# Optimization experiments

Measured on AMD Instinct MI355X. Metric: run time of the kernel, lower is better.

The kernel has to match this reference:

```python
import jax, jax.numpy as jnp
import numpy as np

LAMDA = 0.5
TEMPERATURE = 0.07
EPS = 1e-5


def setup_inputs() -> dict:
    key = jax.random.key(0)
    k1, k2, k3 = jax.random.split(key, 3)
    N, D = 8192, 128
    features = jax.random.normal(k1, (N, D), dtype=jnp.float32)
    labels = jax.random.randint(k2, (N,), 0, 100, dtype=jnp.int64 if jax.config.jax_enable_x64 else jnp.int32)
    domain_labels = jax.random.randint(k3, (N,), 0, 4, dtype=jnp.int64 if jax.config.jax_enable_x64 else jnp.int32)
    return {"features": features, "labels": labels, "domain_labels": domain_labels}


def reference(features, labels, domain_labels):
    N = features.shape[0]
    # L2-normalize rows (torch.nn.functional.normalize, eps=1e-12)
    norms = jnp.maximum(jnp.linalg.norm(features, axis=1, keepdims=True), 1e-12)
    f = features / norms
    sim = jnp.matmul(f, f.T) / TEMPERATURE  # [N, N]

    same_label = labels[:, None] == labels[None, :]
    same_dom = domain_labels[:, None] == domain_labels[None, :]
    offdiag = ~jnp.eye(N, dtype=bool)

    # per-pair domain weight: lamda in-domain, (1-lamda) out-of-domain
    w_exp = jnp.where(same_dom, LAMDA, 1.0 - LAMDA) * jnp.exp(sim)

    # denominator: all off-diagonal pairs (positives + negatives), weighted
    denom = jnp.sum(jnp.where(offdiag, w_exp, 0.0), axis=1) + EPS  # [N]

    pos = same_label & offdiag
    log_frac = jnp.log(w_exp / denom[:, None] + EPS)
    num_pos = jnp.sum(pos, axis=1)  # [N]
    loss_i = jnp.sum(jnp.where(pos, log_frac, 0.0), axis=1) / jnp.maximum(num_pos, 1)

    # anchors with zero positives produce NaN in torch and are skipped
    valid = num_pos > 0
    nans = jnp.sum(~valid)
    loss = -jnp.sum(jnp.where(valid, loss_i, 0.0))
    return loss / (N - nans + 1)
```

## Files before the change

### kernel.cpp

```cpp
#include <hip/hip_runtime.h>

#define NROWS 8192
#define DDIM  128
#define NBLK  (NROWS / 128)
#define NLAB  100
#define GCAP  160
#define GSPL  2
#define GTPB  5
#define EPSV  1e-5f
#define LN2F  0.69314718055994530942f
#define FSCALE 4.53981643f

typedef short s16x8 __attribute__((ext_vector_type(8)));
typedef float f32x4 __attribute__((ext_vector_type(4)));
typedef unsigned short u16;
typedef unsigned int u32;

__device__ __forceinline__ u16 f2bf(float x) {
  u32 b = __builtin_bit_cast(u32, x);
  u32 r = (b + 0x7FFFu + ((b >> 16) & 1u)) >> 16;
  return (u16)r;
}

__global__ __launch_bounds__(256) void norm_kernel(
    const float* __restrict__ feat, u16* __restrict__ g,
    float* __restrict__ denom) {
  int wave = threadIdx.x >> 6;
  int lane = threadIdx.x & 63;
  int row = (blockIdx.x << 2) + wave;
  const float* fr = feat + (size_t)row * DDIM + (lane << 1);
  float2 v = *(const float2*)fr;
  float ss = v.x * v.x + v.y * v.y;
#pragma unroll
  for (int m = 1; m < 64; m <<= 1) ss += __shfl_xor(ss, m);
  float inv = FSCALE / fmaxf(sqrtf(ss), 1e-12f);
  ushort2 o;
  o.x = f2bf(v.x * inv);
  o.y = f2bf(v.y * inv);
  *(ushort2*)(g + (size_t)row * DDIM + (lane << 1)) = o;
  if (lane == 0) denom[row] = 0.0f;
}

__global__ __launch_bounds__(1024) void bucket_kernel(
    const int* __restrict__ lab, int* __restrict__ offs,
    int* __restrict__ cnts, int* __restrict__ rowlist,
    float* __restrict__ Lsum) {
  __shared__ int h[NLAB], cur[NLAB], off[NLAB];
  int tid = threadIdx.x;
  if (tid < NLAB) h[tid] = 0;
  if (tid == 1023) *Lsum = 0.0f;
  __syncthreads();
  for (int i = tid; i < NROWS; i += 1024) atomicAdd(&h[lab[i]], 1);
  __syncthreads();
  if (tid == 0) {
    int s = 0;
    for (int l = 0; l < NLAB; ++l) { off[l] = s; s += h[l]; }
  }
  __syncthreads();
  if (tid < NLAB) { cur[tid] = off[tid]; offs[tid] = off[tid]; cnts[tid] = h[tid]; }
  __syncthreads();
  for (int i = tid; i < NROWS; i += 1024) {
    int p = atomicAdd(&cur[lab[i]], 1);
    rowlist[p] = i;
  }
}

#define LOADB_TO(bv, BsArr, jt)                                              \
  _Pragma("unroll")                                                          \
  for (int kc = 0; kc < 4; ++kc) {                                           \
    const int c_ = (kc << 2) + lh;                                           \
    bv[kc] = *(const s16x8*)(&BsArr[(size_t)((jt)*16 + lr) * DDIM +          \
                                    ((c_ ^ (lr & 7)) << 3)]);                \
  }

#define MFMA_TO(accv, bv, init0, init1)                                      \
  accv[0] = init0; accv[1] = init1;                                          \
  __builtin_amdgcn_s_setprio(1);                                             \
  _Pragma("unroll")                                                          \
  for (int kc = 0; kc < 4; ++kc) {                                           \
    accv[0] = __builtin_amdgcn_mfma_f32_16x16x32_bf16(a[0][kc], bv[kc],      \
                                                      accv[0], 0, 0, 0);     \
    accv[1] = __builtin_amdgcn_mfma_f32_16x16x32_bf16(a[1][kc], bv[kc],      \
                                                      accv[1], 0, 0, 0);     \
  }                                                                          \
  __builtin_amdgcn_s_setprio(0);

#define EPI_T(accv, jt)                                                      \
  {                                                                          \
    const int tj0 = j0 + (jt)*16;                                            \
    float csum = 0.f;                                                        \
    if (diagblk) {                                                           \
      _Pragma("unroll")                                                      \
      for (int rf = 0; rf < 2; ++rf)                                         \
      _Pragma("unroll")                                                      \
        for (int r = 0; r < 4; ++r) {                                        \
          float e_ = __builtin_amdgcn_exp2f(accv[rf][r]);                    \
          e_ = (gibase[rf] + r == tj0 + lr) ? 0.0f : e_;                     \
          dacc[rf][r] += e_;                                                 \
        }                                                                    \
    } else {                                                                 \
      _Pragma("unroll")                                                      \
      for (int rf = 0; rf < 2; ++rf)                                         \
      _Pragma("unroll")                                                      \
        for (int r = 0; r < 4; ++r) {                                        \
          float e_ = __builtin_amdgcn_exp2f(accv[rf][r]);                    \
          dacc[rf][r] += e_;                                                 \
          csum += e_;                                                        \
        }                                                                    \
      csum += __shfl_xor(csum, 16);                                          \
      csum += __shfl_xor(csum, 32);                                          \
      ccol[jt] = csum;                                                       \
    }                                                                        \
  }

__global__ __launch_bounds__(256, 4) void denom_tri(
    const u16* __restrict__ g, float* __restrict__ denom) {
  const int bi = blockIdx.x, bj = blockIdx.y;
  if (bj < bi) return;
  __shared__ u16 Bs[128 * DDIM];
  const int tid = threadIdx.x;
  const int wave = tid >> 6, lane = tid & 63;
  const int lr = lane & 15, lh = lane >> 4;
  const int i0 = bi * 128 + wave * 32;
  const int j0 = bj * 128;
  const bool diagblk = (bi == bj);

  {
    const int cs = (tid & 15) ^ ((tid >> 4) & 7);
#pragma unroll
    for (int k = 0; k < 8; ++k) {
      const u16* src = g + (size_t)(j0 + k * 16 + (tid >> 4)) * DDIM + (cs << 3);
      u16* dst = &Bs[(size_t)(k * 16 + (wave << 2)) * DDIM];
      __builtin_amdgcn_global_load_lds(
          (const __attribute__((address_space(1))) void*)src,
          (__attribute__((address_space(3))) void*)dst, 16, 0, 0);
    }
  }

  s16x8 a[2][4];
#pragma unroll
  for (int rf = 0; rf < 2; ++rf) {
    const u16* gr = g + (size_t)(i0 + rf * 16 + lr) * DDIM + lh * 8;
#pragma unroll
    for (int kc = 0; kc < 4; ++kc) a[rf][kc] = *(const s16x8*)(gr + kc * 32);
  }
  const int gibase[2] = {i0 + lh * 4, i0 + 16 + lh * 4};

  asm volatile("s_waitcnt vmcnt(0)" ::: "memory");
  __builtin_amdgcn_s_barrier();

  float dacc[2][4] = {};
  float ccol[8] = {};
  const f32x4 m1 = f32x4{-1.f, -1.f, -1.f, -1.f};

  s16x8 b0[4], b1[4];
  f32x4 acc0[2], acc1[2];

  LOADB_TO(b0, Bs, 0)
  MFMA_TO(acc0, b0, m1, m1)
#pragma unroll
  for (int p = 0; p < 3; ++p) {
    LOADB_TO(b1, Bs, 2 * p + 1)
    MFMA_TO(acc1, b1, m1, m1)
    EPI_T(acc0, 2 * p)
    LOADB_TO(b0, Bs, 2 * p + 2)
    MFMA_TO(acc0, b0, m1, m1)
    EPI_T(acc1, 2 * p + 1)
  }
  LOADB_TO(b1, Bs, 7)
  MFMA_TO(acc1, b1, m1, m1)
  EPI_T(acc0, 6)
  EPI_T(acc1, 7)

#pragma unroll
  for (int rf = 0; rf < 2; ++rf)
#pragma unroll
    for (int r = 0; r < 4; ++r) {
      float v = dacc[rf][r];
      v += __shfl_xor(v, 1); v += __shfl_xor(v, 2);
      v += __shfl_xor(v, 4); v += __shfl_xor(v, 8);
      if (lr == 0) atomicAdd(&denom[gibase[rf] + r], v);
    }
  if (!diagblk) {
#pragma unroll
    for (int jt = 0; jt < 8; ++jt)
      if (lane < 16) atomicAdd(&denom[j0 + jt * 16 + lane], ccol[jt]);
  }
}

__global__ __launch_bounds__(320) void group_loss(
    const u16* __restrict__ g, const int* __restrict__ offs,
    const int* __restrict__ cnts, const int* __restrict__ rowlist,
    const float* __restrict__ denom, float* __restrict__ Lsum) {
  __shared__ u16 Bs[GTPB * 16 * DDIM];
  const int lb = blockIdx.x;
  const int z = blockIdx.y;
  const int cnt = cnts[lb];
  if (cnt < 2) return;
  if (z * 16 >= cnt) return;
  const int off = offs[lb];
  const int tid = threadIdx.x;
  const int wave = tid >> 6, lane = tid & 63;
  const int lr = lane & 15, lh = lane >> 4;

#pragma unroll
  for (int s = 0; s < 4; ++s) {
    const int m = s * 320 + tid;
    const int rloc = m >> 4, cc = m & 15;
    const int jt_l = rloc >> 4, rr = rloc & 15;
    const int gidx = (jt_l * GSPL + z) * 16 + rr;
    const int cs = cc ^ (rloc & 7);
    const int grow = rowlist[off + (gidx < cnt ? gidx : 0)];
    const u16* src = g + (size_t)grow * DDIM + (cs << 3);
    u16* dst = &Bs[(size_t)(s * 320 + wave * 64) * 8];
    __builtin_amdgcn_global_load_lds(
        (const __attribute__((address_space(1))) void*)src,
        (__attribute__((address_space(3))) void*)dst, 16, 0, 0);
  }

  s16x8 a[2][4];
#pragma unroll
  for (int rf = 0; rf < 2; ++rf) {
    const int ar = wave * 32 + rf * 16 + lr;
    const int gar = rowlist[off + (ar < cnt ? ar : 0)];
    const u16* gr = g + (size_t)gar * DDIM + lh * 8;
#pragma unroll
    for (int kc = 0; kc < 4; ++kc) a[rf][kc] = *(const s16x8*)(gr + kc * 32);
  }
  const int erow[2] = {wave * 32 + lh * 4, wave * 32 + 16 + lh * 4};
  f32x4 cinit[2];
#pragma unroll
  for (int rf = 0; rf < 2; ++rf)
#pragma unroll
    for (int r = 0; r < 4; ++r) {
      const int er = erow[rf] + r;
      const int gi = rowlist[off + (er < cnt ? er : 0)];
      cinit[rf][r] = -__builtin_amdgcn_logf(denom[gi] + EPSV) - 1.0f;
    }

  asm volatile("s_waitcnt vmcnt(0)" ::: "memory");
  __builtin_amdgcn_s_barrier();

  float lacc[2][4] = {};

#pragma unroll
  for (int jt = 0; jt < GTPB; ++jt) {
    s16x8 b[4];
    LOADB_TO(b, Bs, jt)
    f32x4 acc[2];
    MFMA_TO(acc, b, cinit[0], cinit[1])
    const int col = (jt * GSPL + z) * 16 + lr;
    const bool colok = (col < cnt);
#pragma unroll
    for (int rf = 0; rf < 2; ++rf)
#pragma unroll
      for (int r = 0; r < 4; ++r) {
        const int er = erow[rf] + r;
        const bool valid = colok && (er < cnt) && (er != col);
        float x = __builtin_amdgcn_exp2f(acc[rf][r]) + EPSV;
        float lf = __builtin_amdgcn_logf(x);
        lacc[rf][r] += valid ? lf : 0.0f;
      }
  }

  const float scale = LN2F / (float)(cnt - 1);
  float wtot = 0.f;
#pragma unroll
  for (int rf = 0; rf < 2; ++rf)
#pragma unroll
    for (int r = 0; r < 4; ++r) {
      float v = lacc[rf][r];
      v += __shfl_xor(v, 1); v += __shfl_xor(v, 2);
      v += __shfl_xor(v, 4); v += __shfl_xor(v, 8);
      const int er = erow[rf] + r;
      if (lr == 0 && er < cnt) wtot += v * scale;
    }
  wtot += __shfl_xor(wtot, 1);  wtot += __shfl_xor(wtot, 2);
  wtot += __shfl_xor(wtot, 4);  wtot += __shfl_xor(wtot, 8);
  wtot += __shfl_xor(wtot, 16); wtot += __shfl_xor(wtot, 32);
  if (lane == 0 && wtot != 0.0f) atomicAdd(Lsum, wtot);
}

__global__ __launch_bounds__(64) void final_kernel(
    const int* __restrict__ cnts, const float* __restrict__ Lsum,
    float* __restrict__ out) {
  int lane = threadIdx.x;
  int v = 0;
  if (lane < NLAB) { int c = cnts[lane]; v += (c > 1) ? c : 0; }
  if (lane + 64 < NLAB) { int c = cnts[lane + 64]; v += (c > 1) ? c : 0; }
  v += __shfl_xor(v, 1);  v += __shfl_xor(v, 2);
  v += __shfl_xor(v, 4);  v += __shfl_xor(v, 8);
  v += __shfl_xor(v, 16); v += __shfl_xor(v, 32);
  if (lane == 0) out[0] = -Lsum[0] / (float)(v + 1);
}

extern "C" void kernel_launch(void* const* d_in, const int* in_sizes, int n_in,
                              void* d_out, int out_size, void* d_ws, size_t ws_size,
                              hipStream_t stream) {
  const float* feat = (const float*)d_in[0];
  const int* labels = (const int*)d_in[1];
  float* out = (float*)d_out;

  char* ws = (char*)d_ws;
  u16* g        = (u16*)(ws);
  float* denom  = (float*)(ws + (2u << 20));
  int* offs     = (int*)(ws + (2u << 20) + 32768);
  int* cnts     = (int*)(ws + (2u << 20) + 33280);
  float* Lsum   = (float*)(ws + (2u << 20) + 33792);
  int* rowlist  = (int*)(ws + (2u << 20) + 65536);

  norm_kernel<<<NROWS / 4, 256, 0, stream>>>(feat, g, denom);
  bucket_kernel<<<1, 1024, 0, stream>>>(labels, offs, cnts, rowlist, Lsum);
  denom_tri<<<dim3(NBLK, NBLK), 256, 0, stream>>>(g, denom);
  group_loss<<<dim3(NLAB, GSPL), 320, 0, stream>>>(g, offs, cnts, rowlist, denom, Lsum);
  final_kernel<<<1, 64, 0, stream>>>(cnts, Lsum, out);
}
```

Baseline: 59.94 us.

## Fold bucketing into denom kernel and final reduction into group_loss

Removes two of five kernel launches. The label histogram and row-list bucketing now run inside block (0,0) of the denominator kernel, and the final normalization is done by the last-finishing group_loss block using an atomic completion counter. This cuts launch gaps and serialization, but block (0,0) now carries extra serial work that may lengthen the critical path of denom_tri. The completion counter also relies on a threadfence and atomic ordering being correct.

```diff
diff --git a/kernel.cpp b/kernel.cpp
--- a/kernel.cpp
+++ b/kernel.cpp
@@ -24,7 +24,8 @@
 
 __global__ __launch_bounds__(256) void norm_kernel(
     const float* __restrict__ feat, u16* __restrict__ g,
-    float* __restrict__ denom) {
+    float* __restrict__ denom, float* __restrict__ Lsum,
+    int* __restrict__ dcount) {
   int wave = threadIdx.x >> 6;
   int lane = threadIdx.x & 63;
   int row = (blockIdx.x << 2) + wave;
@@ -39,30 +40,7 @@
   o.y = f2bf(v.y * inv);
   *(ushort2*)(g + (size_t)row * DDIM + (lane << 1)) = o;
   if (lane == 0) denom[row] = 0.0f;
-}
-
-__global__ __launch_bounds__(1024) void bucket_kernel(
-    const int* __restrict__ lab, int* __restrict__ offs,
-    int* __restrict__ cnts, int* __restrict__ rowlist,
-    float* __restrict__ Lsum) {
-  __shared__ int h[NLAB], cur[NLAB], off[NLAB];
-  int tid = threadIdx.x;
-  if (tid < NLAB) h[tid] = 0;
-  if (tid == 1023) *Lsum = 0.0f;
-  __syncthreads();
-  for (int i = tid; i < NROWS; i += 1024) atomicAdd(&h[lab[i]], 1);
-  __syncthreads();
-  if (tid == 0) {
-    int s = 0;
-    for (int l = 0; l < NLAB; ++l) { off[l] = s; s += h[l]; }
-  }
-  __syncthreads();
-  if (tid < NLAB) { cur[tid] = off[tid]; offs[tid] = off[tid]; cnts[tid] = h[tid]; }
-  __syncthreads();
-  for (int i = tid; i < NROWS; i += 1024) {
-    int p = atomicAdd(&cur[lab[i]], 1);
-    rowlist[p] = i;
-  }
+  if (blockIdx.x == 0 && threadIdx.x == 0) { *Lsum = 0.0f; *dcount = 0; }
 }
 
 #define LOADB_TO(bv, BsArr, jt)                                              \
@@ -114,10 +92,13 @@
   }
 
 __global__ __launch_bounds__(256, 4) void denom_tri(
-    const u16* __restrict__ g, float* __restrict__ denom) {
+    const u16* __restrict__ g, float* __restrict__ denom,
+    const int* __restrict__ lab, int* __restrict__ offs,
+    int* __restrict__ cnts, int* __restrict__ rowlist) {
   const int bi = blockIdx.x, bj = blockIdx.y;
   if (bj < bi) return;
   __shared__ u16 Bs[128 * DDIM];
+  __shared__ int h[NLAB], cur[NLAB], off[NLAB];
   const int tid = threadIdx.x;
   const int wave = tid >> 6, lane = tid & 63;
   const int lr = lane & 15, lh = lane >> 4;
@@ -145,6 +126,24 @@
     for (int kc = 0; kc < 4; ++kc) a[rf][kc] = *(const s16x8*)(gr + kc * 32);
   }
   const int gibase[2] = {i0 + lh * 4, i0 + 16 + lh * 4};
+
+  if (bi == 0 && bj == 0) {
+    if (tid < NLAB) h[tid] = 0;
+    __syncthreads();
+    for (int i = tid; i < NROWS; i += 256) atomicAdd(&h[lab[i]], 1);
+    __syncthreads();
+    if (tid == 0) {
+      int s = 0;
+      for (int l = 0; l < NLAB; ++l) { off[l] = s; s += h[l]; }
+    }
+    __syncthreads();
+    if (tid < NLAB) { cur[tid] = off[tid]; offs[tid] = off[tid]; cnts[tid] = h[tid]; }
+    __syncthreads();
+    for (int i = tid; i < NROWS; i += 256) {
+      int p = atomicAdd(&cur[lab[i]], 1);
+      rowlist[p] = i;
+    }
+  }
 
   asm volatile("s_waitcnt vmcnt(0)" ::: "memory");
   __builtin_amdgcn_s_barrier();
@@ -191,107 +190,108 @@
 __global__ __launch_bounds__(320) void group_loss(
     const u16* __restrict__ g, const int* __restrict__ offs,
     const int* __restrict__ cnts, const int* __restrict__ rowlist,
-    const float* __restrict__ denom, float* __restrict__ Lsum) {
+    const float* __restrict__ denom, float* __restrict__ Lsum,
+    int* __restrict__ dcount, float* __restrict__ out) {
   __shared__ u16 Bs[GTPB * 16 * DDIM];
   const int lb = blockIdx.x;
   const int z = blockIdx.y;
   const int cnt = cnts[lb];
-  if (cnt < 2) return;
-  if (z * 16 >= cnt) return;
   const int off = offs[lb];
   const int tid = threadIdx.x;
   const int wave = tid >> 6, lane = tid & 63;
   const int lr = lane & 15, lh = lane >> 4;
-
-#pragma unroll
-  for (int s = 0; s < 4; ++s) {
-    const int m = s * 320 + tid;
-    const int rloc = m >> 4, cc = m & 15;
-    const int jt_l = rloc >> 4, rr = rloc & 15;
-    const int gidx = (jt_l * GSPL + z) * 16 + rr;
-    const int cs = cc ^ (rloc & 7);
-    const int grow = rowlist[off + (gidx < cnt ? gidx : 0)];
-    const u16* src = g + (size_t)grow * DDIM + (cs << 3);
-    u16* dst = &Bs[(size_t)(s * 320 + wave * 64) * 8];
-    __builtin_amdgcn_global_load_lds(
-        (const __attribute__((address_space(1))) void*)src,
-        (__attribute__((address_space(3))) void*)dst, 16, 0, 0);
-  }
-
-  s16x8 a[2][4];
-#pragma unroll
-  for (int rf = 0; rf < 2; ++rf) {
-    const int ar = wave * 32 + rf * 16 + lr;
-    const int gar = rowlist[off + (ar < cnt ? ar : 0)];
-    const u16* gr = g + (size_t)gar * DDIM + lh * 8;
-#pragma unroll
-    for (int kc = 0; kc < 4; ++kc) a[rf][kc] = *(const s16x8*)(gr + kc * 32);
-  }
-  const int erow[2] = {wave * 32 + lh * 4, wave * 32 + 16 + lh * 4};
-  f32x4 cinit[2];
-#pragma unroll
-  for (int rf = 0; rf < 2; ++rf)
-#pragma unroll
-    for (int r = 0; r < 4; ++r) {
-      const int er = erow[rf] + r;
-      const int gi = rowlist[off + (er < cnt ? er : 0)];
-      cinit[rf][r] = -__builtin_amdgcn_logf(denom[gi] + EPSV) - 1.0f;
-    }
-
-  asm volatile("s_waitcnt vmcnt(0)" ::: "memory");
-  __builtin_amdgcn_s_barrier();
-
-  float lacc[2][4] = {};
-
-#pragma unroll
-  for (int jt = 0; jt < GTPB; ++jt) {
-    s16x8 b[4];
-    LOADB_TO(b, Bs, jt)
-    f32x4 acc[2];
-    MFMA_TO(acc, b, cinit[0], cinit[1])
-    const int col = (jt * GSPL + z) * 16 + lr;
-    const bool colok = (col < cnt);
+  const bool active = (cnt >= 2) && (z * 16 < cnt);
+
+  if (active) {
+#pragma unroll
+    for (int s = 0; s < 4; ++s) {
+      const int m = s * 320 + tid;
+      const int rloc = m >> 4, cc = m & 15;
+      const int jt_l = rloc >> 4, rr = rloc & 15;
+      const int gidx = (jt_l * GSPL + z) * 16 + rr;
+      const int cs = cc ^ (rloc & 7);
+      const int grow = rowlist[off + (gidx < cnt ? gidx : 0)];
+      const u16* src = g + (size_t)grow * DDIM + (cs << 3);
+      u16* dst = &Bs[(size_t)(s * 320 + wave * 64) * 8];
+      __builtin_amdgcn_global_load_lds(
+          (const __attribute__((address_space(1))) void*)src,
+          (__attribute__((address_space(3))) void*)dst, 16, 0, 0);
+    }
+
+    s16x8 a[2][4];
+#pragma unroll
+    for (int rf = 0; rf < 2; ++rf) {
+      const int ar = wave * 32 + rf * 16 + lr;
+      const int gar = rowlist[off + (ar < cnt ? ar : 0)];
+      const u16* gr = g + (size_t)gar * DDIM + lh * 8;
+#pragma unroll
+      for (int kc = 0; kc < 4; ++kc) a[rf][kc] = *(const s16x8*)(gr + kc * 32);
+    }
+    const int erow[2] = {wave * 32 + lh * 4, wave * 32 + 16 + lh * 4};
+    f32x4 cinit[2];
 #pragma unroll
     for (int rf = 0; rf < 2; ++rf)
 #pragma unroll
       for (int r = 0; r < 4; ++r) {
         const int er = erow[rf] + r;
-        const bool valid = colok && (er < cnt) && (er != col);
-        float x = __builtin_amdgcn_exp2f(acc[rf][r]) + EPSV;
-        float lf = __builtin_amdgcn_logf(x);
-        lacc[rf][r] += valid ? lf : 0.0f;
+        const int gi = rowlist[off + (er < cnt ? er : 0)];
+        cinit[rf][r] = -__builtin_amdgcn_logf(denom[gi] + EPSV) - 1.0f;
       }
-  }
-
-  const float scale = LN2F / (float)(cnt - 1);
-  float wtot = 0.f;
-#pragma unroll
-  for (int rf = 0; rf < 2; ++rf)
-#pragma unroll
-    for (int r = 0; r < 4; ++r) {
-      float v = lacc[rf][r];
-      v += __shfl_xor(v, 1); v += __shfl_xor(v, 2);
-      v += __shfl_xor(v, 4); v += __shfl_xor(v, 8);
-      const int er = erow[rf] + r;
-      if (lr == 0 && er < cnt) wtot += v * scale;
-    }
-  wtot += __shfl_xor(wtot, 1);  wtot += __shfl_xor(wtot, 2);
-  wtot += __shfl_xor(wtot, 4);  wtot += __shfl_xor(wtot, 8);
-  wtot += __shfl_xor(wtot, 16); wtot += __shfl_xor(wtot, 32);
-  if (lane == 0 && wtot != 0.0f) atomicAdd(Lsum, wtot);
-}
-
-__global__ __launch_bounds__(64) void final_kernel(
-    const int* __restrict__ cnts, const float* __restrict__ Lsum,
-    float* __restrict__ out) {
-  int lane = threadIdx.x;
-  int v = 0;
-  if (lane < NLAB) { int c = cnts[lane]; v += (c > 1) ? c : 0; }
-  if (lane + 64 < NLAB) { int c = cnts[lane + 64]; v += (c > 1) ? c : 0; }
-  v += __shfl_xor(v, 1);  v += __shfl_xor(v, 2);
-  v += __shfl_xor(v, 4);  v += __shfl_xor(v, 8);
-  v += __shfl_xor(v, 16); v += __shfl_xor(v, 32);
-  if (lane == 0) out[0] = -Lsum[0] / (float)(v + 1);
+
+    asm volatile("s_waitcnt vmcnt(0)" ::: "memory");
+    __builtin_amdgcn_s_barrier();
+
+    float lacc[2][4] = {};
+
+#pragma unroll
+    for (int jt = 0; jt < GTPB; ++jt) {
+      s16x8 b[4];
+      LOADB_TO(b, Bs, jt)
+      f32x4 acc[2];
+      MFMA_TO(acc, b, cinit[0], cinit[1])
+      const int col = (jt * GSPL + z) * 16 + lr;
+      const bool colok = (col < cnt);
+#pragma unroll
+      for (int rf = 0; rf < 2; ++rf)
+#pragma unroll
+        for (int r = 0; r < 4; ++r) {
+          const int er = erow[rf] + r;
+          const bool valid = colok && (er < cnt) && (er != col);
+          float x = __builtin_amdgcn_exp2f(acc[rf][r]) + EPSV;
+          float lf = __builtin_amdgcn_logf(x);
+          lacc[rf][r] += valid ? lf : 0.0f;
+        }
+    }
+
+    const float scale = LN2F / (float)(cnt - 1);
+    float wtot = 0.f;
+#pragma unroll
+    for (int rf = 0; rf < 2; ++rf)
+#pragma unroll
+      for (int r = 0; r < 4; ++r) {
+        float v = lacc[rf][r];
+        v += __shfl_xor(v, 1); v += __shfl_xor(v, 2);
+        v += __shfl_xor(v, 4); v += __shfl_xor(v, 8);
+        const int er = erow[rf] + r;
+        if (lr == 0 && er < cnt) wtot += v * scale;
+      }
+    wtot += __shfl_xor(wtot, 1);  wtot += __shfl_xor(wtot, 2);
+    wtot += __shfl_xor(wtot, 4);  wtot += __shfl_xor(wtot, 8);
+    wtot += __shfl_xor(wtot, 16); wtot += __shfl_xor(wtot, 32);
+    if (lane == 0 && wtot != 0.0f) atomicAdd(Lsum, wtot);
+  }
+
+  __threadfence();
+  __syncthreads();
+  if (tid == 0) {
+    int done = atomicAdd(dcount, 1);
+    if (done == NLAB * GSPL - 1) {
+      float L = atomicAdd(Lsum, 0.0f);
+      int v = 0;
+      for (int l = 0; l < NLAB; ++l) { int c = cnts[l]; v += (c > 1) ? c : 0; }
+      out[0] = -L / (float)(v + 1);
+    }
+  }
 }
 
 extern "C" void kernel_launch(void* const* d_in, const int* in_sizes, int n_in,
@@ -307,11 +307,11 @@
   int* offs     = (int*)(ws + (2u << 20) + 32768);
   int* cnts     = (int*)(ws + (2u << 20) + 33280);
   float* Lsum   = (float*)(ws + (2u << 20) + 33792);
+  int* dcount   = (int*)(ws + (2u << 20) + 33796);
   int* rowlist  = (int*)(ws + (2u << 20) + 65536);
 
-  norm_kernel<<<NROWS / 4, 256, 0, stream>>>(feat, g, denom);
-  bucket_kernel<<<1, 1024, 0, stream>>>(labels, offs, cnts, rowlist, Lsum);
-  denom_tri<<<dim3(NBLK, NBLK), 256, 0, stream>>>(g, denom);
-  group_loss<<<dim3(NLAB, GSPL), 320, 0, stream>>>(g, offs, cnts, rowlist, denom, Lsum);
-  final_kernel<<<1, 64, 0, stream>>>(cnts, Lsum, out);
-}
+  norm_kernel<<<NROWS / 4, 256, 0, stream>>>(feat, g, denom, Lsum, dcount);
+  denom_tri<<<dim3(NBLK, NBLK), 256, 0, stream>>>(g, denom, labels, offs, cnts, rowlist);
+  group_loss<<<dim3(NLAB, GSPL), 320, 0, stream>>>(g, offs, cnts, rowlist, denom,
+                                                   Lsum, dcount, out);
+}
```

After: 66.21 us. +10.5%, slower.
